# Kernel optimization log

Measured on AMD Instinct MI355X. Metric: run time of the kernel, lower is better.

## Reference

```python
import jax, jax.numpy as jnp
import numpy as np

B = 4096
D_IN = 1024
H1 = 2048
H2 = 1024
E = 7          # num_experts, forced by broadcasting in source
T = 2          # num_tasks
NS = 7         # scene dimension of S
EMB_ROWS = 10
EMB_DIM = 16


def setup_inputs() -> dict:
    key = jax.random.key(0)
    ks = jax.random.split(key, 8)
    x = jax.random.normal(ks[0], (B, D_IN), dtype=jnp.float32)
    scene = jax.random.randint(ks[1], (B,), 0, E)
    # Expert MLP params, stacked over experts: Linear(D_IN->H1)+ReLU, Linear(H1->H2)+ReLU
    W1 = jax.random.normal(ks[2], (E, D_IN, H1), dtype=jnp.float32) * (1.0 / np.sqrt(D_IN))
    b1 = jnp.zeros((E, H1), dtype=jnp.float32)
    W2 = jax.random.normal(ks[3], (E, H1, H2), dtype=jnp.float32) * (1.0 / np.sqrt(H1))
    b2 = jnp.zeros((E, H2), dtype=jnp.float32)
    # Routing tensor S: [7, input_dim+16, num_experts] (xavier-like init)
    S = jax.random.normal(ks[4], (NS, D_IN + EMB_DIM, E), dtype=jnp.float32) * 0.02
    scene_emb = jax.random.normal(ks[5], (EMB_ROWS, EMB_DIM), dtype=jnp.float32)
    return {"x": x, "scene": scene, "W1": W1, "b1": b1, "W2": W2, "b2": b2,
            "S": S, "scene_emb": scene_emb}


def _forward(x, scene, W1, b1, W2, b2, S, scene_emb):
    # Experts (vectorized over the E expert MLPs): [B,E,H2]
    h = jax.nn.relu(jnp.einsum('bd,edh->beh', x, W1) + b1)
    experts_out = jax.nn.relu(jnp.einsum('beh,eho->beo', h, W2) + b2)

    se = scene_emb[scene]                       # [B,16]
    xc = jnp.concatenate([x, se], axis=-1)      # [B, D_IN+16]
    G = jnp.einsum('bd,sde->bse', xc, S)        # [B, 7, E]
    G = jnp.transpose(G, (0, 2, 1))             # [B, E, 7]
    G = jax.nn.softmax(G, axis=-1)

    logG = jnp.log(G)                           # [B, E, 7]
    q = jnp.sum(jnp.log(G * 7.0) / 7.0, axis=-1)  # [B, E]

    KG = jnp.eye(E, dtype=x.dtype)
    ses = KG[scene][:, None, :]                 # [B, 1, E]

    _, pi = jax.lax.top_k(jnp.sum(ses * logG, axis=-1), 6)  # [B,6]
    _, qi = jax.lax.top_k(q, 6)                              # [B,6]
    select = ((KG[pi].sum(axis=1) + KG[qi].sum(axis=1)) > 0).astype(x.dtype)  # [B,E]

    gate = jax.nn.softmax(jnp.sum(G * ses, axis=-1), axis=-1) * select  # [B,E]
    out = jnp.einsum('be,bed->bd', gate, experts_out)                    # [B,H2]
    # self.gate ModuleList is unused in the source forward; each task output is identical
    return jnp.stack([out] * T, axis=0)         # [T, B, H2]


def reference(x, scene, W1, b1, W2, b2, S, scene_emb):
    return _forward(x, scene, W1, b1, W2, b2, S, scene_emb)
```

## Files before the change

kernel.cpp:

```cpp
#include <hip/hip_runtime.h>
#include <hip/hip_bf16.h>

typedef unsigned short u16;
typedef __bf16 bf8 __attribute__((ext_vector_type(8)));
typedef float f4 __attribute__((ext_vector_type(4)));

__device__ __forceinline__ u16 f2bf(float f) {
    unsigned int u = __float_as_uint(f);
    u = (u + 0x7fffu + ((u >> 16) & 1u)) >> 16;
    return (u16)u;
}

__device__ __forceinline__ void gload16(const u16* g, u16* l) {
    __builtin_amdgcn_global_load_lds((const __attribute__((address_space(1))) void*)g,
                                     (__attribute__((address_space(3))) void*)l, 16, 0, 0);
}

__global__ void cvt_x_kernel(const float* __restrict__ in, u16* __restrict__ out, int n4) {
    int i = blockIdx.x * blockDim.x + threadIdx.x;
    int stride = gridDim.x * blockDim.x;
    for (; i < n4; i += stride) {
        float4 v = ((const float4*)in)[i];
        ushort4 o;
        o.x = f2bf(v.x); o.y = f2bf(v.y); o.z = f2bf(v.z); o.w = f2bf(v.w);
        ((ushort4*)out)[i] = o;
    }
}

__global__ void transpose_cvt_kernel(const float* __restrict__ in, u16* __restrict__ out,
                                     int R, int C) {
    __shared__ float t[32][33];
    int e = blockIdx.z;
    int c0 = blockIdx.x * 32, r0 = blockIdx.y * 32;
    int tx = threadIdx.x & 31, ty = threadIdx.x >> 5;
    const float* ip = in + (size_t)e * R * C;
    u16* op = out + (size_t)e * R * C;
#pragma unroll
    for (int k = 0; k < 32; k += 8)
        t[ty + k][tx] = ip[(size_t)(r0 + ty + k) * C + c0 + tx];
    __syncthreads();
#pragma unroll
    for (int k = 0; k < 32; k += 8)
        op[(size_t)(c0 + ty + k) * R + r0 + tx] = f2bf(t[tx][ty + k]);
}

__global__ void transpose_S_kernel(const float* __restrict__ S, float* __restrict__ ST) {
    int idx = blockIdx.x * 256 + threadIdx.x;
    if (idx >= 1040 * 52) return;
    int d = idx / 52, c = idx % 52;
    ST[idx] = (c < 49) ? S[(c / 7) * 7280 + d * 7 + (c % 7)] : 0.f;
}

__global__ void gating_kernel(const float* __restrict__ x, const int* __restrict__ scene,
                              const float* __restrict__ ST, const float* __restrict__ semb,
                              float* __restrict__ gate) {
    __shared__ float xc[4][1040];
    __shared__ float Lsh[4][49];
    int wv = threadIdx.x >> 6, lane = threadIdx.x & 63;
    int row = blockIdx.x * 4 + wv;
    float* xcw = xc[wv];
    const float* xr = x + (size_t)row * 1024;
    for (int d = lane; d < 1024; d += 64) xcw[d] = xr[d];
    int sc = scene[row];
    if (lane < 16) xcw[1024 + lane] = semb[sc * 16 + lane];
    __syncthreads();

    if (lane < 49) {
        const float* STp = ST + lane;
        float a0 = 0.f, a1 = 0.f, a2 = 0.f, a3 = 0.f;
        for (int d = 0; d < 1040; d += 4) {
            a0 += xcw[d]     * STp[d * 52];
            a1 += xcw[d + 1] * STp[d * 52 + 52];
            a2 += xcw[d + 2] * STp[d * 52 + 104];
            a3 += xcw[d + 3] * STp[d * 52 + 156];
        }
        Lsh[wv][lane] = (a0 + a1) + (a2 + a3);
    }
    __syncthreads();

    if (lane == 0) {
        float logG[7][7], Gsc[7], piS[7], qS[7];
        for (int e = 0; e < 7; e++) {
            float L[7];
            float m = -1e30f;
            for (int s = 0; s < 7; s++) { L[s] = Lsh[wv][s * 7 + e]; m = fmaxf(m, L[s]); }
            float sum = 0.f;
            for (int s = 0; s < 7; s++) sum += expf(L[s] - m);
            float lse = m + logf(sum);
            float qs = 0.f;
            for (int s = 0; s < 7; s++) { logG[e][s] = L[s] - lse; qs += logG[e][s]; }
            piS[e] = logG[e][sc];
            qS[e] = qs;
            Gsc[e] = expf(logG[e][sc]);
        }
        int epi = 0, eqi = 0; float bp = piS[0], bq = qS[0];
        for (int e = 1; e < 7; e++) {
            if (piS[e] <= bp) { bp = piS[e]; epi = e; }
            if (qS[e]  <= bq) { bq = qS[e];  eqi = e; }
        }
        float mg = -1e30f;
        for (int e = 0; e < 7; e++) mg = fmaxf(mg, Gsc[e]);
        float sum = 0.f;
        float ex[7];
        for (int e = 0; e < 7; e++) { ex[e] = expf(Gsc[e] - mg); sum += ex[e]; }
        float inv = 1.f / sum;
        for (int e = 0; e < 7; e++) {
            float g = ex[e] * inv;
            if (e == epi && e == eqi) g = 0.f;
            gate[row * 7 + e] = g;
        }
    }
}

template<bool G2>
__global__ __launch_bounds__(512, 2) void gemm8p_kernel(
    const u16* __restrict__ Abase, const u16* __restrict__ Bbase,
    const float* __restrict__ bias, const float* __restrict__ gate,
    void* __restrict__ outp)
{
    constexpr int M = 4096;
    constexpr int K = G2 ? 2048 : 1024;
    constexpr int N = G2 ? 1024 : 2048;
    constexpr int NT = K / 64;
    constexpr int LOG2NT = G2 ? 5 : 4;

    extern __shared__ u16 lds[];

    const int tid = threadIdx.x;
    const int lane = tid & 63;
    const int wid = tid >> 6;
    const int wr = wid >> 2, wc = wid & 3;
    const int ln15 = lane & 15, lnk = (lane >> 4) * 8;

    int bm, bn, e0, nE, grp;
    if constexpr (G2) {
        int id = blockIdx.x;
        int xcd = id & 7, slot = id >> 3;
        grp = xcd & 1;
        bn = slot & 3;
        bm = (slot >> 2) * 4 + (xcd >> 1);
        e0 = grp * 4; nE = grp ? 3 : 4;
    } else {
        int id = blockIdx.x;
        e0 = id >> 8;
        bm = (id & 255) >> 3;
        bn = id & 7;
        nE = 1; grp = 0;
    }
    const int NTtot = nE * NT;

    const int sr = tid >> 3;
    const int sc = (tid & 7) * 8;

    auto stageA = [&](int gt, int buf) {
#pragma unroll
        for (int l = 0; l < 2; ++l) {
            int r = l * 64 + sr;
            int cs = sc ^ ((r & 7) << 3);
            const u16* g = Abase + (G2 ? (size_t)(e0 + (gt >> LOG2NT)) * M * K : (size_t)0)
                         + (size_t)(bm * 128 + r) * K + (gt & (NT - 1)) * 64 + cs;
            gload16(g, lds + buf * 24576 + l * 4096 + tid * 8);
        }
    };
    auto stageB = [&](int gt, int buf, int h) {
#pragma unroll
        for (int l = 0; l < 2; ++l) {
            int rb = h * 128 + l * 64 + sr;
            int cs = sc ^ ((rb & 7) << 3);
            const u16* g = Bbase + (size_t)(e0 + (gt >> LOG2NT)) * N * K
                         + (size_t)(bn * 256 + rb) * K + (gt & (NT - 1)) * 64 + cs;
            gload16(g, lds + buf * 24576 + 8192 + h * 8192 + l * 4096 + tid * 8);
        }
    };
    auto aoff = [&](int mi, int ks) {
        int r = wr * 64 + mi * 16 + ln15;
        int c = ks * 32 + lnk;
        return r * 64 + (c ^ ((r & 7) << 3));
    };
    auto boff = [&](int ni, int ks) {
        int rb = wc * 64 + ni * 16 + ln15;
        int c = ks * 32 + lnk;
        return rb * 64 + (c ^ ((rb & 7) << 3));
    };

    f4 acc[4][4] = {};
    f4 fin[4][4] = {};
    bf8 aA[2][2], bL[2][2], bH[2][2];

    stageA(0, 0); stageB(0, 0, 0); stageB(0, 0, 1);

    for (int gt = 0; gt < NTtot; ++gt) {
        const int cur = gt & 1, nxt = cur ^ 1;
        const bool more = (gt + 1 < NTtot);
        const u16* Ac = lds + cur * 24576;
        const u16* Bc = lds + cur * 24576 + 8192;
        if (more) {
            stageA(gt + 1, nxt); stageB(gt + 1, nxt, 0);
            asm volatile("s_waitcnt vmcnt(4)" ::: "memory");
        } else {
            asm volatile("s_waitcnt vmcnt(0)" ::: "memory");
        }
        __builtin_amdgcn_sched_barrier(0);
        __builtin_amdgcn_s_barrier();
        __builtin_amdgcn_sched_barrier(0);
#pragma unroll
        for (int mi = 0; mi < 2; ++mi)
#pragma unroll
            for (int ks = 0; ks < 2; ++ks)
                aA[mi][ks] = *(const bf8*)(Ac + aoff(mi, ks));
#pragma unroll
        for (int ni = 0; ni < 2; ++ni)
#pragma unroll
            for (int ks = 0; ks < 2; ++ks)
                bL[ni][ks] = *(const bf8*)(Bc + boff(ni, ks));
        asm volatile("s_waitcnt lgkmcnt(0)" ::: "memory");
        __builtin_amdgcn_sched_barrier(0);
        __builtin_amdgcn_s_setprio(1);
#pragma unroll
        for (int mi = 0; mi < 2; ++mi)
#pragma unroll
            for (int ni = 0; ni < 2; ++ni)
#pragma unroll
                for (int ks = 0; ks < 2; ++ks)
                    acc[mi][ni] = __builtin_amdgcn_mfma_f32_16x16x32_bf16(aA[mi][ks], bL[ni][ks], acc[mi][ni], 0, 0, 0);
        __builtin_amdgcn_s_setprio(0);
        if (more) stageB(gt + 1, nxt, 1);
#pragma unroll
        for (int ni = 0; ni < 2; ++ni)
#pragma unroll
            for (int ks = 0; ks < 2; ++ks)
                bH[ni][ks] = *(const bf8*)(Bc + boff(2 + ni, ks));
        asm volatile("s_waitcnt lgkmcnt(0)" ::: "memory");
        __builtin_amdgcn_sched_barrier(0);
        __builtin_amdgcn_s_setprio(1);
#pragma unroll
        for (int mi = 0; mi < 2; ++mi)
#pragma unroll
            for (int ni = 0; ni < 2; ++ni)
#pragma unroll
                for (int ks = 0; ks < 2; ++ks)
                    acc[mi][2 + ni] = __builtin_amdgcn_mfma_f32_16x16x32_bf16(aA[mi][ks], bH[ni][ks], acc[mi][2 + ni], 0, 0, 0);
        __builtin_amdgcn_s_setprio(0);
#pragma unroll
        for (int mi = 0; mi < 2; ++mi)
#pragma unroll
            for (int ks = 0; ks < 2; ++ks)
                aA[mi][ks] = *(const bf8*)(Ac + aoff(2 + mi, ks));
        asm volatile("s_waitcnt lgkmcnt(0)" ::: "memory");
        __builtin_amdgcn_sched_barrier(0);
        __builtin_amdgcn_s_setprio(1);
#pragma unroll
        for (int mi = 0; mi < 2; ++mi)
#pragma unroll
            for (int ni = 0; ni < 2; ++ni)
#pragma unroll
                for (int ks = 0; ks < 2; ++ks)
                    acc[2 + mi][2 + ni] = __builtin_amdgcn_mfma_f32_16x16x32_bf16(aA[mi][ks], bH[ni][ks], acc[2 + mi][2 + ni], 0, 0, 0);
        __builtin_amdgcn_s_setprio(0);
        __builtin_amdgcn_sched_barrier(0);
        __builtin_amdgcn_s_barrier();
        __builtin_amdgcn_sched_barrier(0);
        __builtin_amdgcn_s_setprio(1);
#pragma unroll
        for (int mi = 0; mi < 2; ++mi)
#pragma unroll
            for (int ni = 0; ni < 2; ++ni)
#pragma unroll
                for (int ks = 0; ks < 2; ++ks)
                    acc[2 + mi][ni] = __builtin_amdgcn_mfma_f32_16x16x32_bf16(aA[mi][ks], bL[ni][ks], acc[2 + mi][ni], 0, 0, 0);
        __builtin_amdgcn_s_setprio(0);
        __builtin_amdgcn_sched_barrier(0);
        if constexpr (G2) {
            if ((gt & (NT - 1)) == NT - 1) {
                int e = e0 + (gt >> LOG2NT);
                float bloc[4];
#pragma unroll
                for (int ni = 0; ni < 4; ++ni)
                    bloc[ni] = bias[e * N + bn * 256 + wc * 64 + ni * 16 + ln15];
#pragma unroll
                for (int mi = 0; mi < 4; ++mi)
#pragma unroll
                    for (int i = 0; i < 4; ++i) {
                        int row = bm * 128 + wr * 64 + mi * 16 + (lane >> 4) * 4 + i;
                        float g = gate[row * 7 + e];
#pragma unroll
                        for (int ni = 0; ni < 4; ++ni) {
                            fin[mi][ni][i] += g * fmaxf(acc[mi][ni][i] + bloc[ni], 0.f);
                            acc[mi][ni][i] = 0.f;
                        }
                    }
            }
        }
    }

    if constexpr (G2) {
        float* po = (float*)outp + (size_t)grp * M * N;
#pragma unroll
        for (int mi = 0; mi < 4; ++mi)
#pragma unroll
            for (int i = 0; i < 4; ++i) {
                size_t row = (size_t)(bm * 128 + wr * 64 + mi * 16 + (lane >> 4) * 4 + i);
#pragma unroll
                for (int ni = 0; ni < 4; ++ni)
                    po[row * N + bn * 256 + wc * 64 + ni * 16 + ln15] = fin[mi][ni][i];
            }
    } else {
        float bloc[4];
#pragma unroll
        for (int ni = 0; ni < 4; ++ni)
            bloc[ni] = bias[e0 * N + bn * 256 + wc * 64 + ni * 16 + ln15];
        u16* Hp = (u16*)outp + (size_t)e0 * M * N;
#pragma unroll
        for (int mi = 0; mi < 4; ++mi)
#pragma unroll
            for (int i = 0; i < 4; ++i) {
                size_t row = (size_t)(bm * 128 + wr * 64 + mi * 16 + (lane >> 4) * 4 + i);
#pragma unroll
                for (int ni = 0; ni < 4; ++ni)
                    Hp[row * N + bn * 256 + wc * 64 + ni * 16 + ln15] =
                        f2bf(fmaxf(acc[mi][ni][i] + bloc[ni], 0.f));
            }
    }
}

__global__ void combine_kernel(const float* __restrict__ p0, const float* __restrict__ p1,
                               float* __restrict__ out, int n4) {
    int i = blockIdx.x * blockDim.x + threadIdx.x;
    int stride = gridDim.x * blockDim.x;
    for (; i < n4; i += stride) {
        float4 a = ((const float4*)p0)[i];
        float4 b = ((const float4*)p1)[i];
        float4 v = make_float4(a.x + b.x, a.y + b.y, a.z + b.z, a.w + b.w);
        ((float4*)out)[i] = v;
        ((float4*)out)[i + n4] = v;
    }
}

extern "C" void kernel_launch(void* const* d_in, const int* in_sizes, int n_in,
                              void* d_out, int out_size, void* d_ws, size_t ws_size,
                              hipStream_t stream) {
    const float* x     = (const float*)d_in[0];
    const int*   scene = (const int*)d_in[1];
    const float* W1    = (const float*)d_in[2];
    const float* b1    = (const float*)d_in[3];
    const float* W2    = (const float*)d_in[4];
    const float* b2    = (const float*)d_in[5];
    const float* S     = (const float*)d_in[6];
    const float* semb  = (const float*)d_in[7];
    float* out = (float*)d_out;

    char* ws = (char*)d_ws;
    float* part = (float*)(ws);
    u16*   xb   = (u16*)(ws);
    u16*   W1T  = (u16*)(ws + 8388608);
    u16*   W2T  = (u16*)(ws + 37748736);
    u16*   Hb   = (u16*)(ws + 67108864);
    float* gate = (float*)(ws + 184549376);
    float* ST   = (float*)(ws + 184664064);

    (void)hipFuncSetAttribute(reinterpret_cast<const void*>(gemm8p_kernel<false>),
                              hipFuncAttributeMaxDynamicSharedMemorySize, 98304);
    (void)hipFuncSetAttribute(reinterpret_cast<const void*>(gemm8p_kernel<true>),
                              hipFuncAttributeMaxDynamicSharedMemorySize, 98304);

    cvt_x_kernel<<<2048, 256, 0, stream>>>(x, xb, 4096 * 1024 / 4);
    transpose_cvt_kernel<<<dim3(64, 32, 7), 256, 0, stream>>>(W1, W1T, 1024, 2048);
    transpose_cvt_kernel<<<dim3(32, 64, 7), 256, 0, stream>>>(W2, W2T, 2048, 1024);
    transpose_S_kernel<<<(1040 * 52 + 255) / 256, 256, 0, stream>>>(S, ST);
    gating_kernel<<<1024, 256, 0, stream>>>(x, scene, ST, semb, gate);
    gemm8p_kernel<false><<<1792, 512, 98304, stream>>>(xb, W1T, b1, nullptr, Hb);
    gemm8p_kernel<true><<<256, 512, 98304, stream>>>(Hb, W2T, b2, gate, part);
    combine_kernel<<<2048, 256, 0, stream>>>(part, part + 4096 * 1024, out, 4096 * 1024 / 4);
}
```

Before: 387.3 us.

## Use 256x256 per-expert GEMM tiles with atomic gated reduction

Both expert GEMMs now use 256x256 output tiles, up from 128x256, so each block covers a single expert. The double-buffered LDS footprint grows to 128KB, and the block index is remapped so consecutive blocks go to different XCDs. The second GEMM no longer loops over groups of experts into fin registers. Each block instead applies bias, ReLU and the gate weight, then atomically adds its result into one zeroed fp32 buffer, so combine becomes a plain copy. This aims for more operand reuse and fewer partial buffers, at the cost of a memset, heavy fp32 atomic traffic, and probably one resident block per CU.

```diff
diff --git a/kernel.cpp b/kernel.cpp
--- a/kernel.cpp
+++ b/kernel.cpp
@@ -113,7 +113,7 @@
 }
 
 template<bool G2>
-__global__ __launch_bounds__(512, 2) void gemm8p_kernel(
+__global__ __launch_bounds__(512, 2) void gemmE_kernel(
     const u16* __restrict__ Abase, const u16* __restrict__ Bbase,
     const float* __restrict__ bias, const float* __restrict__ gate,
     void* __restrict__ outp)
@@ -122,7 +122,7 @@
     constexpr int K = G2 ? 2048 : 1024;
     constexpr int N = G2 ? 1024 : 2048;
     constexpr int NT = K / 64;
-    constexpr int LOG2NT = G2 ? 5 : 4;
+    constexpr int BNT = N / 256;
 
     extern __shared__ u16 lds[];
 
@@ -132,48 +132,38 @@
     const int wr = wid >> 2, wc = wid & 3;
     const int ln15 = lane & 15, lnk = (lane >> 4) * 8;
 
-    int bm, bn, e0, nE, grp;
-    if constexpr (G2) {
-        int id = blockIdx.x;
-        int xcd = id & 7, slot = id >> 3;
-        grp = xcd & 1;
-        bn = slot & 3;
-        bm = (slot >> 2) * 4 + (xcd >> 1);
-        e0 = grp * 4; nE = grp ? 3 : 4;
-    } else {
-        int id = blockIdx.x;
-        e0 = id >> 8;
-        bm = (id & 255) >> 3;
-        bn = id & 7;
-        nE = 1; grp = 0;
-    }
-    const int NTtot = nE * NT;
+    const int nwg = gridDim.x, cpx = nwg >> 3;
+    const int wg = (blockIdx.x & 7) * cpx + (blockIdx.x >> 3);
+    const int e  = wg / (16 * BNT);
+    const int rem = wg % (16 * BNT);
+    const int bm = rem / BNT, bn = rem % BNT;
+
+    const u16* Ae = Abase + (G2 ? (size_t)e * M * K : (size_t)0);
+    const u16* Be = Bbase + (size_t)e * N * K;
 
     const int sr = tid >> 3;
     const int sc = (tid & 7) * 8;
 
-    auto stageA = [&](int gt, int buf) {
-#pragma unroll
-        for (int l = 0; l < 2; ++l) {
+    auto stageA = [&](int kt, int buf) {
+#pragma unroll
+        for (int l = 0; l < 4; ++l) {
             int r = l * 64 + sr;
             int cs = sc ^ ((r & 7) << 3);
-            const u16* g = Abase + (G2 ? (size_t)(e0 + (gt >> LOG2NT)) * M * K : (size_t)0)
-                         + (size_t)(bm * 128 + r) * K + (gt & (NT - 1)) * 64 + cs;
-            gload16(g, lds + buf * 24576 + l * 4096 + tid * 8);
+            const u16* g = Ae + (size_t)(bm * 256 + r) * K + kt * 64 + cs;
+            gload16(g, lds + buf * 32768 + l * 4096 + tid * 8);
         }
     };
-    auto stageB = [&](int gt, int buf, int h) {
+    auto stageB = [&](int kt, int buf, int h) {
 #pragma unroll
         for (int l = 0; l < 2; ++l) {
             int rb = h * 128 + l * 64 + sr;
             int cs = sc ^ ((rb & 7) << 3);
-            const u16* g = Bbase + (size_t)(e0 + (gt >> LOG2NT)) * N * K
-                         + (size_t)(bn * 256 + rb) * K + (gt & (NT - 1)) * 64 + cs;
-            gload16(g, lds + buf * 24576 + 8192 + h * 8192 + l * 4096 + tid * 8);
+            const u16* g = Be + (size_t)(bn * 256 + rb) * K + kt * 64 + cs;
+            gload16(g, lds + buf * 32768 + 16384 + h * 8192 + l * 4096 + tid * 8);
         }
     };
     auto aoff = [&](int mi, int ks) {
-        int r = wr * 64 + mi * 16 + ln15;
+        int r = wr * 128 + mi * 16 + ln15;
         int c = ks * 32 + lnk;
         return r * 64 + (c ^ ((r & 7) << 3));
     };
@@ -183,19 +173,18 @@
         return rb * 64 + (c ^ ((rb & 7) << 3));
     };
 
-    f4 acc[4][4] = {};
-    f4 fin[4][4] = {};
-    bf8 aA[2][2], bL[2][2], bH[2][2];
+    f4 acc[8][4] = {};
+    bf8 aA[4][2], bL[2][2], bH[2][2];
 
     stageA(0, 0); stageB(0, 0, 0); stageB(0, 0, 1);
 
-    for (int gt = 0; gt < NTtot; ++gt) {
+    for (int gt = 0; gt < NT; ++gt) {
         const int cur = gt & 1, nxt = cur ^ 1;
-        const bool more = (gt + 1 < NTtot);
-        const u16* Ac = lds + cur * 24576;
-        const u16* Bc = lds + cur * 24576 + 8192;
+        const bool more = (gt + 1 < NT);
+        const u16* Ac = lds + cur * 32768;
+        const u16* Bc = lds + cur * 32768 + 16384;
         if (more) {
-            stageA(gt + 1, nxt); stageB(gt + 1, nxt, 0);
+            stageA(gt + 1, nxt);
             asm volatile("s_waitcnt vmcnt(4)" ::: "memory");
         } else {
             asm volatile("s_waitcnt vmcnt(0)" ::: "memory");
@@ -204,7 +193,7 @@
         __builtin_amdgcn_s_barrier();
         __builtin_amdgcn_sched_barrier(0);
 #pragma unroll
-        for (int mi = 0; mi < 2; ++mi)
+        for (int mi = 0; mi < 4; ++mi)
 #pragma unroll
             for (int ks = 0; ks < 2; ++ks)
                 aA[mi][ks] = *(const bf8*)(Ac + aoff(mi, ks));
@@ -217,14 +206,14 @@
         __builtin_amdgcn_sched_barrier(0);
         __builtin_amdgcn_s_setprio(1);
 #pragma unroll
-        for (int mi = 0; mi < 2; ++mi)
+        for (int mi = 0; mi < 4; ++mi)
 #pragma unroll
             for (int ni = 0; ni < 2; ++ni)
 #pragma unroll
                 for (int ks = 0; ks < 2; ++ks)
                     acc[mi][ni] = __builtin_amdgcn_mfma_f32_16x16x32_bf16(aA[mi][ks], bL[ni][ks], acc[mi][ni], 0, 0, 0);
         __builtin_amdgcn_s_setprio(0);
-        if (more) stageB(gt + 1, nxt, 1);
+        if (more) stageB(gt + 1, nxt, 0);
 #pragma unroll
         for (int ni = 0; ni < 2; ++ni)
 #pragma unroll
@@ -234,87 +223,70 @@
         __builtin_amdgcn_sched_barrier(0);
         __builtin_amdgcn_s_setprio(1);
 #pragma unroll
-        for (int mi = 0; mi < 2; ++mi)
+        for (int mi = 0; mi < 4; ++mi)
 #pragma unroll
             for (int ni = 0; ni < 2; ++ni)
 #pragma unroll
                 for (int ks = 0; ks < 2; ++ks)
                     acc[mi][2 + ni] = __builtin_amdgcn_mfma_f32_16x16x32_bf16(aA[mi][ks], bH[ni][ks], acc[mi][2 + ni], 0, 0, 0);
         __builtin_amdgcn_s_setprio(0);
-#pragma unroll
-        for (int mi = 0; mi < 2; ++mi)
+        if (more) stageB(gt + 1, nxt, 1);
+#pragma unroll
+        for (int mi = 0; mi < 4; ++mi)
 #pragma unroll
             for (int ks = 0; ks < 2; ++ks)
-                aA[mi][ks] = *(const bf8*)(Ac + aoff(2 + mi, ks));
+                aA[mi][ks] = *(const bf8*)(Ac + aoff(4 + mi, ks));
         asm volatile("s_waitcnt lgkmcnt(0)" ::: "memory");
         __builtin_amdgcn_sched_barrier(0);
         __builtin_amdgcn_s_setprio(1);
 #pragma unroll
-        for (int mi = 0; mi < 2; ++mi)
+        for (int mi = 0; mi < 4; ++mi)
 #pragma unroll
             for (int ni = 0; ni < 2; ++ni)
 #pragma unroll
                 for (int ks = 0; ks < 2; ++ks)
-                    acc[2 + mi][2 + ni] = __builtin_amdgcn_mfma_f32_16x16x32_bf16(aA[mi][ks], bH[ni][ks], acc[2 + mi][2 + ni], 0, 0, 0);
+                    acc[4 + mi][2 + ni] = __builtin_amdgcn_mfma_f32_16x16x32_bf16(aA[mi][ks], bH[ni][ks], acc[4 + mi][2 + ni], 0, 0, 0);
         __builtin_amdgcn_s_setprio(0);
         __builtin_amdgcn_sched_barrier(0);
         __builtin_amdgcn_s_barrier();
         __builtin_amdgcn_sched_barrier(0);
         __builtin_amdgcn_s_setprio(1);
 #pragma unroll
-        for (int mi = 0; mi < 2; ++mi)
+        for (int mi = 0; mi < 4; ++mi)
 #pragma unroll
             for (int ni = 0; ni < 2; ++ni)
 #pragma unroll
                 for (int ks = 0; ks < 2; ++ks)
-                    acc[2 + mi][ni] = __builtin_amdgcn_mfma_f32_16x16x32_bf16(aA[mi][ks], bL[ni][ks], acc[2 + mi][ni], 0, 0, 0);
+                    acc[4 + mi][ni] = __builtin_amdgcn_mfma_f32_16x16x32_bf16(aA[mi][ks], bL[ni][ks], acc[4 + mi][ni], 0, 0, 0);
         __builtin_amdgcn_s_setprio(0);
         __builtin_amdgcn_sched_barrier(0);
-        if constexpr (G2) {
-            if ((gt & (NT - 1)) == NT - 1) {
-                int e = e0 + (gt >> LOG2NT);
-                float bloc[4];
-#pragma unroll
-                for (int ni = 0; ni < 4; ++ni)
-                    bloc[ni] = bias[e * N + bn * 256 + wc * 64 + ni * 16 + ln15];
-#pragma unroll
-                for (int mi = 0; mi < 4; ++mi)
-#pragma unroll
-                    for (int i = 0; i < 4; ++i) {
-                        int row = bm * 128 + wr * 64 + mi * 16 + (lane >> 4) * 4 + i;
-                        float g = gate[row * 7 + e];
-#pragma unroll
-                        for (int ni = 0; ni < 4; ++ni) {
-                            fin[mi][ni][i] += g * fmaxf(acc[mi][ni][i] + bloc[ni], 0.f);
-                            acc[mi][ni][i] = 0.f;
-                        }
-                    }
-            }
-        }
-    }
-
+    }
+
+    float bloc[4];
+#pragma unroll
+    for (int ni = 0; ni < 4; ++ni)
+        bloc[ni] = bias[e * N + bn * 256 + wc * 64 + ni * 16 + ln15];
     if constexpr (G2) {
-        float* po = (float*)outp + (size_t)grp * M * N;
-#pragma unroll
-        for (int mi = 0; mi < 4; ++mi)
+        float* part = (float*)outp;
+#pragma unroll
+        for (int mi = 0; mi < 8; ++mi)
 #pragma unroll
             for (int i = 0; i < 4; ++i) {
-                size_t row = (size_t)(bm * 128 + wr * 64 + mi * 16 + (lane >> 4) * 4 + i);
-#pragma unroll
-                for (int ni = 0; ni < 4; ++ni)
-                    po[row * N + bn * 256 + wc * 64 + ni * 16 + ln15] = fin[mi][ni][i];
+                int row = bm * 256 + wr * 128 + mi * 16 + (lane >> 4) * 4 + i;
+                float g = gate[row * 7 + e];
+#pragma unroll
+                for (int ni = 0; ni < 4; ++ni) {
+                    float v = g * fmaxf(acc[mi][ni][i] + bloc[ni], 0.f);
+                    atomicAdd(&part[(size_t)row * N + bn * 256 + wc * 64 + ni * 16 + ln15], v);
+                }
             }
     } else {
-        float bloc[4];
-#pragma unroll
-        for (int ni = 0; ni < 4; ++ni)
-            bloc[ni] = bias[e0 * N + bn * 256 + wc * 64 + ni * 16 + ln15];
-        u16* Hp = (u16*)outp + (size_t)e0 * M * N;
-#pragma unroll
-        for (int mi = 0; mi < 4; ++mi)
+        u16* Hp = (u16*)outp + (size_t)e * M * N;
+#pragma unroll
+        for (int mi = 0; mi < 8; ++mi)
 #pragma unroll
             for (int i = 0; i < 4; ++i) {
-                size_t row = (size_t)(bm * 128 + wr * 64 + mi * 16 + (lane >> 4) * 4 + i);
+                size_t row = (size_t)(bm * 256 + wr * 128 + mi * 16 + (lane >> 4) * 4 + i);
 #pragma unroll
                 for (int ni = 0; ni < 4; ++ni)
                     Hp[row * N + bn * 256 + wc * 64 + ni * 16 + ln15] =
@@ -323,14 +295,11 @@
     }
 }
 
-__global__ void combine_kernel(const float* __restrict__ p0, const float* __restrict__ p1,
-                               float* __restrict__ out, int n4) {
+__global__ void combine_kernel(const float* __restrict__ part, float* __restrict__ out, int n4) {
     int i = blockIdx.x * blockDim.x + threadIdx.x;
     int stride = gridDim.x * blockDim.x;
     for (; i < n4; i += stride) {
-        float4 a = ((const float4*)p0)[i];
-        float4 b = ((const float4*)p1)[i];
-        float4 v = make_float4(a.x + b.x, a.y + b.y, a.z + b.z, a.w + b.w);
+        float4 v = ((const float4*)part)[i];
         ((float4*)out)[i] = v;
         ((float4*)out)[i + n4] = v;
     }
@@ -358,17 +327,18 @@
     float* gate = (float*)(ws + 184549376);
     float* ST   = (float*)(ws + 184664064);
 
-    (void)hipFuncSetAttribute(reinterpret_cast<const void*>(gemm8p_kernel<false>),
-                              hipFuncAttributeMaxDynamicSharedMemorySize, 98304);
-    (void)hipFuncSetAttribute(reinterpret_cast<const void*>(gemm8p_kernel<true>),
-                              hipFuncAttributeMaxDynamicSharedMemorySize, 98304);
+    (void)hipFuncSetAttribute(reinterpret_cast<const void*>(gemmE_kernel<false>),
+                              hipFuncAttributeMaxDynamicSharedMemorySize, 131072);
+    (void)hipFuncSetAttribute(reinterpret_cast<const void*>(gemmE_kernel<true>),
+                              hipFuncAttributeMaxDynamicSharedMemorySize, 131072);
 
     cvt_x_kernel<<<2048, 256, 0, stream>>>(x, xb, 4096 * 1024 / 4);
     transpose_cvt_kernel<<<dim3(64, 32, 7), 256, 0, stream>>>(W1, W1T, 1024, 2048);
     transpose_cvt_kernel<<<dim3(32, 64, 7), 256, 0, stream>>>(W2, W2T, 2048, 1024);
     transpose_S_kernel<<<(1040 * 52 + 255) / 256, 256, 0, stream>>>(S, ST);
     gating_kernel<<<1024, 256, 0, stream>>>(x, scene, ST, semb, gate);
-    gemm8p_kernel<false><<<1792, 512, 98304, stream>>>(xb, W1T, b1, nullptr, Hb);
-    gemm8p_kernel<true><<<256, 512, 98304, stream>>>(Hb, W2T, b2, gate, part);
-    combine_kernel<<<2048, 256, 0, stream>>>(part, part + 4096 * 1024, out, 4096 * 1024 / 4);
-}
+    gemmE_kernel<false><<<896, 512, 131072, stream>>>(xb, W1T, b1, nullptr, Hb);
+    (void)hipMemsetAsync(part, 0, (size_t)4096 * 1024 * 4, stream);
+    gemmE_kernel<true><<<448, 512, 131072, stream>>>(Hb, W2T, b2, gate, part);
+    combine_kernel<<<2048, 256, 0, stream>>>(part, out, 4096 * 1024 / 4);
+}
```

After: 423.3 us. 1.09x slower.
